# Performance work log

Hardware: AMD Instinct MI355X
Metric: run time of the kernel (lower is better)

## Reference

```python
import jax, jax.numpy as jnp
import numpy as np

EPS = 1e-5
NUM_ROUTING = 2
PC_N, PC_D = 32, 16  # primary capsules: num, dim
SD = 4               # sqrt(caps_dim) for matrix pose


def layer_norm(x, g, b):
    mu = jnp.mean(x, axis=-1, keepdims=True)
    var = jnp.mean((x - mu) ** 2, axis=-1, keepdims=True)
    return (x - mu) * jax.lax.rsqrt(var + EPS) * g + b


def conv2d(x, w, stride, pad):
    return jax.lax.conv_general_dilated(
        x, w, (stride, stride), [(pad, pad), (pad, pad)],
        dimension_numbers=('NCHW', 'OIHW', 'NCHW'))


def unfold_caps(x, k, s):
    # x: [B,N,H,W,D] -> [B,N,k,k,oh,ow,D]  (torch .unfold over H,W)
    H = x.shape[2]
    oh = (H - k) // s + 1
    idx = s * jnp.arange(oh)[:, None] + jnp.arange(k)[None, :]  # [oh,k]
    p = x[:, :, idx]            # [B,N,oh,k,W,D]
    p = p[:, :, :, :, idx]      # [B,N,oh,k,ow,k,D]
    return jnp.transpose(p, (0, 1, 3, 5, 2, 4, 6))


def caps_conv_step(val, w, stride, next_val=None):
    # val: [B,N,H,W,D]; w: [k,k,N,sd,sd,M]; inverted dot-product attention routing
    k, _, N, sd, _, M = w.shape
    u = unfold_caps(val, k, stride)              # [B,N,k,k,oh,ow,D]
    B, _, _, _, oh, ow, D = u.shape
    u = u.reshape(B, N, k, k, oh, ow, sd, sd)
    scale = 1.0 / np.sqrt(float(sd * sd))
    if next_val is None:
        # uniform query_key = softmax(zeros) = 1/M
        nv = jnp.einsum('bnklhwax,klnxdm->bmhwad', u, w) / M
    else:
        nvp = next_val.reshape(B, M, oh, ow, sd, sd)
        qk = jnp.einsum('bnklhwax,klnxdm,bmhwad->bnklmhw', u, w, nvp) * scale
        qk = jax.nn.softmax(qk, axis=4)
        nv = jnp.einsum('bnklmhw,bnklhwax,klnxdm->bmhwad', qk, u, w)
    return nv.reshape(B, M, oh, ow, sd * sd)


def caps_fc_step(val, w, next_val=None):
    # val: [B,n,D]; w: [n,sd,sd,M]
    n, sd, _, M = w.shape
    B = val.shape[0]
    u = val.reshape(B, n, sd, sd)
    scale = 1.0 / np.sqrt(float(sd * sd))
    if next_val is None:
        nv = jnp.einsum('bnax,nxdm->bmad', u, w) / M
    else:
        nvp = next_val.reshape(B, M, sd, sd)
        qk = jnp.einsum('bnax,nxdm,bmad->bnm', u, w, nvp) * scale
        qk = jax.nn.softmax(qk, axis=2)
        nv = jnp.einsum('bnm,bnax,nxdm->bmad', qk, u, w)
    return nv.reshape(B, M, sd * sd)


def _forward(x, bb_w, bb_b, pc_w, ln0_g, ln0_b, caps_w, ln1_g, ln1_b, fc_w, ln2_g, ln2_b):
    # simple backbone: conv stride2 + relu -> [B,128,32,32]
    c = jax.nn.relu(conv2d(x, bb_w, 2, 1) + bb_b[None, :, None, None])
    # primary capsule conv (no bias) -> [B, 512, 16, 16]
    u = conv2d(c, pc_w, 2, 1)
    B, _, H, W = u.shape
    u = jnp.transpose(u, (0, 2, 3, 1)).reshape(B, H, W, PC_N, PC_D)
    u = jnp.transpose(u, (0, 3, 1, 2, 4))  # [B,N,H,W,D]
    val = layer_norm(u, ln0_g, ln0_b)
    # CapsuleCONV layer with sequential routing (num_routing iterations)
    v = layer_norm(caps_conv_step(val, caps_w, 2), ln1_g, ln1_b)
    for _ in range(NUM_ROUTING - 1):
        v = layer_norm(caps_conv_step(val, caps_w, 2, next_val=v), ln1_g, ln1_b)
    # flatten 5D -> [B, M*oh*ow, D] exactly as torch permute(0,4,1,2,3).view(B,D,-1).permute(0,2,1)
    Bv, M, oh, ow, D = v.shape
    fc_in = jnp.transpose(v, (0, 4, 1, 2, 3)).reshape(Bv, D, M * oh * ow)
    fc_in = jnp.transpose(fc_in, (0, 2, 1))
    # final FC capsule layer (class capsules) with sequential routing
    p = layer_norm(caps_fc_step(fc_in, fc_w), ln2_g, ln2_b)
    for _ in range(NUM_ROUTING - 1):
        p = layer_norm(caps_fc_step(fc_in, fc_w, next_val=p), ln2_g, ln2_b)
    return p  # [B, 10, 16] class-capsule poses


def setup_inputs():
    key = jax.random.key(0)
    ks = jax.random.split(key, 5)
    B, C, HW = 64, 3, 64
    BB_OUT = 128
    CC_N, K = 32, 3
    CLS_N = 10
    cc_out = 7
    in_n_fc = CC_N * cc_out * cc_out  # 1568
    inp = {}
    inp['x'] = jax.random.normal(ks[0], (B, C, HW, HW), jnp.float32)
    inp['bb_w'] = jax.random.normal(ks[1], (BB_OUT, C, 3, 3), jnp.float32) * 0.1
    inp['bb_b'] = jnp.zeros((BB_OUT,), jnp.float32)
    inp['pc_w'] = jax.random.normal(ks[2], (PC_N * PC_D, BB_OUT, 3, 3), jnp.float32) * 0.05
    inp['ln0_g'] = jnp.ones((PC_D,), jnp.float32)
    inp['ln0_b'] = jnp.zeros((PC_D,), jnp.float32)
    cc_const = float(np.sqrt(CC_N / (SD * PC_N * K * K)))
    inp['caps_w'] = cc_const * jax.random.normal(ks[3], (K, K, PC_N, SD, SD, CC_N), jnp.float32)
    inp['ln1_g'] = jnp.ones((16,), jnp.float32)
    inp['ln1_b'] = jnp.zeros((16,), jnp.float32)
    fc_const = float(np.sqrt(CLS_N / (SD * in_n_fc)))
    inp['fc_w'] = fc_const * jax.random.normal(ks[4], (in_n_fc, SD, SD, CLS_N), jnp.float32)
    inp['ln2_g'] = jnp.ones((16,), jnp.float32)
    inp['ln2_b'] = jnp.zeros((16,), jnp.float32)
    return inp


def reference(x, bb_w, bb_b, pc_w, ln0_g, ln0_b, caps_w, ln1_g, ln1_b, fc_w, ln2_g, ln2_b):
    return _forward(x, bb_w, bb_b, pc_w, ln0_g, ln0_b, caps_w, ln1_g, ln1_b, fc_w, ln2_g, ln2_b)
```

## Files before the change

kernel.cpp:

```cpp
#include <hip/hip_runtime.h>


#define EPSLN 1e-5f

typedef short  short8 __attribute__((ext_vector_type(8)));
typedef __bf16 bf16x8 __attribute__((ext_vector_type(8)));
typedef float  f32x4  __attribute__((ext_vector_type(4)));

union Frag { short8 s; bf16x8 b; };

__device__ __forceinline__ uint4 pack_bf16_8(float4 a, float4 b) {
    union { __bf16 h[8]; uint4 u; } r;
    r.h[0] = (__bf16)a.x; r.h[1] = (__bf16)a.y;
    r.h[2] = (__bf16)a.z; r.h[3] = (__bf16)a.w;
    r.h[4] = (__bf16)b.x; r.h[5] = (__bf16)b.y;
    r.h[6] = (__bf16)b.z; r.h[7] = (__bf16)b.w;
    return r.u;
}

__device__ __forceinline__ void gld16(const void* g, void* l) {
    __builtin_amdgcn_global_load_lds(
        (const __attribute__((address_space(1))) void*)g,
        (__attribute__((address_space(3))) void*)l, 16, 0, 0);
}

__global__ __launch_bounds__(256) void k_repack_all(
        const float* __restrict__ bw,  float* __restrict__ bwT,
        const float* __restrict__ pw,  __bf16* __restrict__ wbT,
        const float* __restrict__ fw,  float* __restrict__ fwp,
        const float* __restrict__ cw,  __bf16* __restrict__ cw2,
        __bf16* __restrict__ cwB) {
    int blk = blockIdx.x;
    if (blk < 2304) {
        int i = blk * 256 + threadIdx.x;
        int oc = i / 1152, r = i % 1152;
        int ic = r / 9, tap = r % 9;
        wbT[oc * 1152 + tap * 128 + ic] = (__bf16)pw[i];
    } else if (blk < 3284) {
        int i = (blk - 2304) * 256 + threadIdx.x;
        int m = i % 10;
        int d = (i / 10) & 3;
        int x = (i / 40) & 3;
        int n = i / 160;
        fwp[(m * 1568 + n) * 16 + x * 4 + d] = fw[i];
    } else if (blk < 3860) {
        int i = (blk - 3284) * 256 + threadIdx.x;
        int m  = i & 31;
        int d  = (i >> 5) & 3;
        int x  = (i >> 7) & 3;
        int n  = (i >> 9) & 31;
        int kl = i >> 14;
        cw2[(((kl * 32 + n) * 32) + m) * 16 + x * 4 + d] = (__bf16)cw[i];
    } else if (blk < 4436) {
        int i = (blk - 3860) * 256 + threadIdx.x;
        int m  = i & 31;
        int d  = (i >> 5) & 3;
        int x  = (i >> 7) & 3;
        int n  = (i >> 9) & 31;
        int kl = i >> 14;
        cwB[(m * 4 + d) * 1152 + (n * 9 + kl) * 4 + x] = (__bf16)cw[i];
    } else {
        int i = (blk - 4436) * 256 + threadIdx.x;
        if (i < 3456) {
            int oc = i / 27, r = i % 27;
            bwT[r * 128 + oc] = bw[i];
        }
    }
}

__global__ __launch_bounds__(256) void k_conv1(const float* __restrict__ x,
                                               const float* __restrict__ bwT,
                                               const float* __restrict__ bb,
                                               __bf16* __restrict__ c2p) {
    int gid = blockIdx.x * 256 + threadIdx.x;
    int oc4 = gid & 31;
    int p   = gid >> 5;
    int w = p & 31, h = (p >> 5) & 31, b = p >> 10;
    const float* xb = x + b * 12288;
    float4 acc = *(const float4*)(bb + oc4 * 4);
    #pragma unroll
    for (int ky = 0; ky < 3; ++ky) {
        int ih = 2 * h + ky - 1;
        if ((unsigned)ih >= 64u) continue;
        #pragma unroll
        for (int kx = 0; kx < 3; ++kx) {
            int iw = 2 * w + kx - 1;
            if ((unsigned)iw >= 64u) continue;
            #pragma unroll
            for (int ic = 0; ic < 3; ++ic) {
                float in = xb[(ic * 64 + ih) * 64 + iw];
                float4 wv = *(const float4*)(bwT + (ic * 9 + ky * 3 + kx) * 128 + oc4 * 4);
                acc.x = fmaf(in, wv.x, acc.x);
                acc.y = fmaf(in, wv.y, acc.y);
                acc.z = fmaf(in, wv.z, acc.z);
                acc.w = fmaf(in, wv.w, acc.w);
            }
        }
    }
    union { __bf16 h4[4]; unsigned long long ull; } r;
    r.h4[0] = (__bf16)fmaxf(acc.x, 0.f);
    r.h4[1] = (__bf16)fmaxf(acc.y, 0.f);
    r.h4[2] = (__bf16)fmaxf(acc.z, 0.f);
    r.h4[3] = (__bf16)fmaxf(acc.w, 0.f);
    *(unsigned long long*)(c2p + ((b * 34 + h + 1) * 34 + (w + 1)) * 128 + oc4 * 4) = r.ull;
}

__global__ __launch_bounds__(256) void k_conv2_mfma(const __bf16* __restrict__ c2p,
                                                    const __bf16* __restrict__ wbT,
                                                    const float* __restrict__ g,
                                                    const float* __restrict__ bt,
                                                    float* __restrict__ val) {
    __shared__ unsigned short sA[2][128 * 32];
    __shared__ unsigned short sB[2][64 * 32];

    const int t = threadIdx.x;
    const int mblk = blockIdx.x >> 3, nblk = blockIdx.x & 7;
    const int pbase = mblk * 128, ocbase = nblk * 64;
    const int b = pbase >> 8;

    const int kc8 = (t & 3) * 8;
    const int r0 = t >> 2;
    const int oh0 = ((pbase + r0) >> 4) & 15, ow0 = (pbase + r0) & 15;
    const int oh1 = ((pbase + r0 + 64) >> 4) & 15, ow1 = (pbase + r0 + 64) & 15;

    const unsigned short* cb = (const unsigned short*)c2p + (size_t)b * 147968;
    const unsigned short* ws = (const unsigned short*)wbT
                               + (ocbase + (t >> 2)) * 1152 + kc8;

    const int lane = t & 63, wid = t >> 6;
    const int lo = lane & 15, hi = lane >> 4;

    f32x4 acc[2][4];
    #pragma unroll
    for (int fr = 0; fr < 2; ++fr)
        #pragma unroll
        for (int fc = 0; fc < 4; ++fc)
            acc[fr][fc] = (f32x4){0.f, 0.f, 0.f, 0.f};

    auto stage = [&](int buf, int ks) {
        int tap = ks / 4, ic0 = (ks % 4) * 32;
        int ty = tap / 3, tx = tap % 3;
        gld16(cb + ((2 * oh0 + ty) * 34 + (2 * ow0 + tx)) * 128 + ic0 + kc8,
              &sA[buf][(unsigned)t * 8]);
        gld16(cb + ((2 * oh1 + ty) * 34 + (2 * ow1 + tx)) * 128 + ic0 + kc8,
              &sA[buf][((unsigned)t + 256) * 8]);
        gld16(ws + ks * 32, &sB[buf][(unsigned)t * 8]);
    };

    stage(0, 0);
    __syncthreads();

    for (int ks = 0; ks < 36; ++ks) {
        const int cur = ks & 1;
        if (ks + 1 < 36) stage(cur ^ 1, ks + 1);
        Frag af0, af1, bf[4];
        af0.s = *(const short8*)&sA[cur][(wid * 32 + lo) * 32 + hi * 8];
        af1.s = *(const short8*)&sA[cur][(wid * 32 + 16 + lo) * 32 + hi * 8];
        #pragma unroll
        for (int fc = 0; fc < 4; ++fc)
            bf[fc].s = *(const short8*)&sB[cur][(fc * 16 + lo) * 32 + hi * 8];
        #pragma unroll
        for (int fc = 0; fc < 4; ++fc) {
            acc[0][fc] = __builtin_amdgcn_mfma_f32_16x16x32_bf16(
                af0.b, bf[fc].b, acc[0][fc], 0, 0, 0);
            acc[1][fc] = __builtin_amdgcn_mfma_f32_16x16x32_bf16(
                af1.b, bf[fc].b, acc[1][fc], 0, 0, 0);
        }
        __syncthreads();
    }

    const float gv = g[lo], bv = bt[lo];
    #pragma unroll
    for (int fr = 0; fr < 2; ++fr) {
        #pragma unroll
        for (int fc = 0; fc < 4; ++fc) {
            const int n = (ocbase >> 4) + fc;
            #pragma unroll
            for (int j = 0; j < 4; ++j) {
                float v = acc[fr][fc][j];
                float s1 = v, s2 = v * v;
                #pragma unroll
                for (int off = 1; off < 16; off <<= 1) {
                    s1 += __shfl_xor(s1, off);
                    s2 += __shfl_xor(s2, off);
                }
                float mu  = s1 * (1.f / 16.f);
                float var = s2 * (1.f / 16.f) - mu * mu;
                float rs  = rsqrtf(var + EPSLN);
                float o   = (v - mu) * rs * gv + bv;
                int p  = pbase + wid * 32 + fr * 16 + hi * 4 + j;
                int oh = (p >> 4) & 15, ow = p & 15;
                val[(((b * 32 + n) * 16 + oh) * 16 + ow) * 16 + lo] = o;
            }
        }
    }
}

__global__ __launch_bounds__(256) void k_nv1_mfma(const float* __restrict__ val,
                                                  const __bf16* __restrict__ cwB,
                                                  float* __restrict__ nv1g) {
    __shared__ unsigned short sA[128 * 32];
    __shared__ unsigned short sB[64 * 32];

    const int t = threadIdx.x;
    const int mblk = blockIdx.x >> 1, nblk = blockIdx.x & 1;
    const int pbase = mblk * 128, ocbase = nblk * 64;

    const float* vbase[2];
    #pragma unroll
    for (int u = 0; u < 2; ++u) {
        int r = pbase + (t >> 2) + u * 64;
        int site = r >> 2, a = r & 3;
        int b = site / 49, hw = site % 49;
        int h = hw / 7, w = hw % 7;
        vbase[u] = val + (size_t)b * 131072 + (2 * h) * 256 + (2 * w) * 16 + a * 4;
    }
    const unsigned short* wsrc = (const unsigned short*)cwB
                                 + (ocbase + (t >> 2)) * 1152 + (t & 3) * 8;

    const int lane = t & 63, wid = t >> 6;
    const int lo = lane & 15, hi = lane >> 4;

    f32x4 acc[2][4];
    #pragma unroll
    for (int fr = 0; fr < 2; ++fr)
        #pragma unroll
        for (int fc = 0; fc < 4; ++fc)
            acc[fr][fc] = (f32x4){0.f, 0.f, 0.f, 0.f};

    auto itemoff = [](int i) {
        int n = i / 9, kl = i % 9;
        return n * 4096 + (kl / 3) * 256 + (kl % 3) * 16;
    };

    {
        int i0 = (t & 3) * 2;
        int o0 = itemoff(i0), o1 = itemoff(i0 + 1);
        uint4 a0 = pack_bf16_8(*(const float4*)(vbase[0] + o0),
                               *(const float4*)(vbase[0] + o1));
        uint4 a1 = pack_bf16_8(*(const float4*)(vbase[1] + o0),
                               *(const float4*)(vbase[1] + o1));
        uint4 b0 = *(const uint4*)(wsrc);
        *(uint4*)&sA[(unsigned)t * 8]         = a0;
        *(uint4*)&sA[((unsigned)t + 256) * 8] = a1;
        *(uint4*)&sB[(unsigned)t * 8]         = b0;
        __syncthreads();
    }

    for (int ks = 0; ks < 36; ++ks) {
        uint4 a0, a1, b0;
        const bool pre = (ks + 1) < 36;
        if (pre) {
            int i0 = (ks + 1) * 8 + (t & 3) * 2;
            int o0 = itemoff(i0), o1 = itemoff(i0 + 1);
            a0 = pack_bf16_8(*(const float4*)(vbase[0] + o0),
                             *(const float4*)(vbase[0] + o1));
            a1 = pack_bf16_8(*(const float4*)(vbase[1] + o0),
                             *(const float4*)(vbase[1] + o1));
            b0 = *(const uint4*)(wsrc + (ks + 1) * 32);
        }
        Frag af0, af1, bf[4];
        af0.s = *(const short8*)&sA[(wid * 32 + lo) * 32 + hi * 8];
        af1.s = *(const short8*)&sA[(wid * 32 + 16 + lo) * 32 + hi * 8];
        #pragma unroll
        for (int fc = 0; fc < 4; ++fc)
            bf[fc].s = *(const short8*)&sB[(fc * 16 + lo) * 32 + hi * 8];
        #pragma unroll
        for (int fc = 0; fc < 4; ++fc) {
            acc[0][fc] = __builtin_amdgcn_mfma_f32_16x16x32_bf16(
                af0.b, bf[fc].b, acc[0][fc], 0, 0, 0);
            acc[1][fc] = __builtin_amdgcn_mfma_f32_16x16x32_bf16(
                af1.b, bf[fc].b, acc[1][fc], 0, 0, 0);
        }
        __syncthreads();
        if (pre) {
            *(uint4*)&sA[(unsigned)t * 8]         = a0;
            *(uint4*)&sA[((unsigned)t + 256) * 8] = a1;
            *(uint4*)&sB[(unsigned)t * 8]         = b0;
        }
        __syncthreads();
    }

    #pragma unroll
    for (int fr = 0; fr < 2; ++fr)
        #pragma unroll
        for (int fc = 0; fc < 4; ++fc)
            #pragma unroll
            for (int j = 0; j < 4; ++j) {
                int row = pbase + wid * 32 + fr * 16 + hi * 4 + j;
                int col = ocbase + fc * 16 + lo;
                nv1g[row * 128 + col] = acc[fr][fc][j];
            }
}

__global__ __launch_bounds__(256) void k_capsfused(const float* __restrict__ val,
                                                   const __bf16* __restrict__ cw2,
                                                   const float* __restrict__ nv1g,
                                                   const float* __restrict__ g,
                                                   const float* __restrict__ bt,
                                                   float* __restrict__ vout) {
    int bb = blockIdx.x / 49;
    int hw = blockIdx.x % 49;
    int h = hw / 7, w = hw % 7;

    __shared__ float4 uloc4[2][1152];
    __shared__ float  v1s[2][512];
    float* wred = (float*)uloc4;

    for (int t = threadIdx.x; t < 2304; t += 256) {
        int s  = t >= 1152;
        int tt = t - s * 1152;
        int f  = tt & 3;
        int kl = (tt >> 2) % 9;
        int n  = tt / 36;
        int k = kl / 3, l = kl % 3;
        int b = bb + s * 32;
        uloc4[s][tt] = *(const float4*)(val +
            (((b * 32 + n) * 16 + (2 * h + k)) * 16 + (2 * w + l)) * 16 + f * 4);
    }

    const int lane  = threadIdx.x & 31;
    const int grpid = threadIdx.x >> 5;
    const int wid   = threadIdx.x >> 6;
    const bool half0 = (threadIdx.x & 32) == 0;

    float nvp[2][16];
    #pragma unroll
    for (int s = 0; s < 2; ++s) {
        int site = (bb + s * 32) * 49 + hw;
        #pragma unroll
        for (int a = 0; a < 4; ++a) {
            float4 q = *(const float4*)(nv1g + (site * 4 + a) * 128 + lane * 4);
            nvp[s][a * 4 + 0] = q.x * (1.f / 32.f);
            nvp[s][a * 4 + 1] = q.y * (1.f / 32.f);
            nvp[s][a * 4 + 2] = q.z * (1.f / 32.f);
            nvp[s][a * 4 + 3] = q.w * (1.f / 32.f);
        }
        float mu = 0.f;
        #pragma unroll
        for (int j = 0; j < 16; ++j) mu += nvp[s][j];
        mu *= (1.f / 16.f);
        float var = 0.f;
        #pragma unroll
        for (int j = 0; j < 16; ++j) { float d = nvp[s][j] - mu; var += d * d; }
        var *= (1.f / 16.f);
        float rs = rsqrtf(var + EPSLN);
        #pragma unroll
        for (int j = 0; j < 16; ++j)
            nvp[s][j] = (nvp[s][j] - mu) * rs * g[j] + bt[j];
    }

    float nvacc[2][16];
    #pragma unroll
    for (int s = 0; s < 2; ++s)
        #pragma unroll
        for (int j = 0; j < 16; ++j) nvacc[s][j] = 0.f;

    __syncthreads();

    {
        uint4 wq0, wq1;
        {
            int n = grpid / 9, kl = grpid % 9;
            const uint4* wb = (const uint4*)(cw2 + (((kl * 32 + n) * 32) + lane) * 16);
            wq0 = wb[0]; wq1 = wb[1];
        }
        for (int it = grpid; it < 288; it += 8) {
            int nit = it + 8;
            uint4 nq0 = wq0, nq1 = wq1;
            if (nit < 288) {
                int n = nit / 9, kl = nit % 9;
                const uint4* wb = (const uint4*)(cw2 + (((kl * 32 + n) * 32) + lane) * 16);
                nq0 = wb[0]; nq1 = wb[1];
            }
            float cwv[16];
            {
                union { uint4 u; __bf16 hh[8]; } qa, qb;
                qa.u = wq0; qb.u = wq1;
                #pragma unroll
                for (int j = 0; j < 8; ++j) {
                    cwv[j] = (float)qa.hh[j]; cwv[8 + j] = (float)qb.hh[j];
                }
            }
            #pragma unroll
            for (int s = 0; s < 2; ++s) {
                float u16[16];
                #pragma unroll
                for (int f = 0; f < 4; ++f) {
                    float4 t4 = uloc4[s][it * 4 + f];
                    u16[f * 4 + 0] = t4.x; u16[f * 4 + 1] = t4.y;
                    u16[f * 4 + 2] = t4.z; u16[f * 4 + 3] = t4.w;
                }
                float votes[16];
                #pragma unroll
                for (int a = 0; a < 4; ++a)
                    #pragma unroll
                    for (int d = 0; d < 4; ++d) {
                        float v = 0.f;
                        #pragma unroll
                        for (int x = 0; x < 4; ++x)
                            v = fmaf(u16[a * 4 + x], cwv[x * 4 + d], v);
                        votes[a * 4 + d] = v;
                    }
                float qk = 0.f;
                #pragma unroll
                for (int j = 0; j < 16; ++j) qk = fmaf(votes[j], nvp[s][j], qk);
                qk *= 0.25f;
                float e = __expf(fminf(qk, 60.f));
                float sm = e;
                #pragma unroll
                for (int off = 1; off < 32; off <<= 1) sm += __shfl_xor(sm, off);
                float qv = e * __builtin_amdgcn_rcpf(sm);
                #pragma unroll
                for (int j = 0; j < 16; ++j) nvacc[s][j] = fmaf(qv, votes[j], nvacc[s][j]);
            }
            wq0 = nq0; wq1 = nq1;
        }
    }

    #pragma unroll
    for (int s = 0; s < 2; ++s)
        #pragma unroll
        for (int j = 0; j < 16; ++j)
            nvacc[s][j] += __shfl_xor(nvacc[s][j], 32);
    #pragma unroll
    for (int s = 0; s < 2; ++s) {
        __syncthreads();
        if (half0) {
            #pragma unroll
            for (int j = 0; j < 16; ++j) wred[wid * 544 + lane * 17 + j] = nvacc[s][j];
        }
        __syncthreads();
        for (int o = threadIdx.x; o < 512; o += 256) {
            int mm = o >> 4, j = o & 15;
            float sum = wred[0 * 544 + mm * 17 + j] + wred[1 * 544 + mm * 17 + j]
                      + wred[2 * 544 + mm * 17 + j] + wred[3 * 544 + mm * 17 + j];
            v1s[s][o] = sum;
        }
    }
    __syncthreads();
    if (threadIdx.x < 64) {
        int s = threadIdx.x >> 5, m = threadIdx.x & 31;
        int b = bb + s * 32;
        float v16[16], mu = 0.f;
        #pragma unroll
        for (int j = 0; j < 16; ++j) { v16[j] = v1s[s][m * 16 + j]; mu += v16[j]; }
        mu *= (1.f / 16.f);
        float var = 0.f;
        #pragma unroll
        for (int j = 0; j < 16; ++j) { float t = v16[j] - mu; var += t * t; }
        var *= (1.f / 16.f);
        float rs = rsqrtf(var + EPSLN);
        float o16[16];
        #pragma unroll
        for (int j = 0; j < 16; ++j) o16[j] = (v16[j] - mu) * rs * g[j] + bt[j];
        float4* dst = (float4*)(vout + (((b * 32 + m) * 7 + h) * 7 + w) * 16);
        dst[0] = make_float4(o16[0],  o16[1],  o16[2],  o16[3]);
        dst[1] = make_float4(o16[4],  o16[5],  o16[6],  o16[7]);
        dst[2] = make_float4(o16[8],  o16[9],  o16[10], o16[11]);
        dst[3] = make_float4(o16[12], o16[13], o16[14], o16[15]);
    }
}

__global__ __launch_bounds__(256) void k_fc1(const float* __restrict__ fin,
                                             const float* __restrict__ fwp,
                                             const float* __restrict__ g,
                                             const float* __restrict__ bt,
                                             float* __restrict__ p) {
    int b = blockIdx.x / 10, m = blockIdx.x % 10;
    const float* fb = fin + b * 1568 * 16;
    const float* wb = fwp + m * 1568 * 16;
    float acc[16];
    #pragma unroll
    for (int j = 0; j < 16; ++j) acc[j] = 0.f;

    for (int n = threadIdx.x; n < 1568; n += 256) {
        const float4* u4 = (const float4*)(fb + n * 16);
        const float4* w4 = (const float4*)(wb + n * 16);
        float u16[16], w16[16];
        #pragma unroll
        for (int f = 0; f < 4; ++f) {
            float4 a = u4[f], bq = w4[f];
            u16[f * 4 + 0] = a.x;  u16[f * 4 + 1] = a.y;
            u16[f * 4 + 2] = a.z;  u16[f * 4 + 3] = a.w;
            w16[f * 4 + 0] = bq.x; w16[f * 4 + 1] = bq.y;
            w16[f * 4 + 2] = bq.z; w16[f * 4 + 3] = bq.w;
        }
        #pragma unroll
        for (int a = 0; a < 4; ++a)
            #pragma unroll
            for (int d = 0; d < 4; ++d) {
                float s = acc[a * 4 + d];
                #pragma unroll
                for (int x = 0; x < 4; ++x)
                    s = fmaf(u16[a * 4 + x], w16[x * 4 + d], s);
                acc[a * 4 + d] = s;
            }
    }
    #pragma unroll
    for (int j = 0; j < 16; ++j)
        #pragma unroll
        for (int off = 1; off < 64; off <<= 1)
            acc[j] += __shfl_xor(acc[j], off);

    __shared__ float red[4][16];
    int wid = threadIdx.x >> 6, ln = threadIdx.x & 63;
    if (ln == 0) {
        #pragma unroll
        for (int j = 0; j < 16; ++j) red[wid][j] = acc[j];
    }
    __syncthreads();
    if (threadIdx.x < 16) {
        int j = threadIdx.x;
        float s = (red[0][j] + red[1][j] + red[2][j] + red[3][j]) * 0.1f;
        float mu = s;
        #pragma unroll
        for (int off = 1; off < 16; off <<= 1) mu += __shfl_xor(mu, off);
        mu *= (1.f / 16.f);
        float t = s - mu;
        float var = t * t;
        #pragma unroll
        for (int off = 1; off < 16; off <<= 1) var += __shfl_xor(var, off);
        var *= (1.f / 16.f);
        float rs = rsqrtf(var + EPSLN);
        p[(b * 10 + m) * 16 + j] = t * rs * g[j] + bt[j];
    }
}

__global__ __launch_bounds__(256) void k_fc2_part(const float* __restrict__ fin,
                                                  const float* __restrict__ fw,
                                                  const float* __restrict__ p,
                                                  float* __restrict__ part) {
    int b = blockIdx.x >> 4, slice = blockIdx.x & 15;
    int ad    = threadIdx.x & 15;
    int grpid = threadIdx.x >> 4;
    int a = ad >> 2, d = ad & 3;

    float pv[10];
    #pragma unroll
    for (int m = 0; m < 10; ++m) pv[m] = p[(b * 10 + m) * 16 + ad];

    float acc[10];
    #pragma unroll
    for (int m = 0; m < 10; ++m) acc[m] = 0.f;

    const float* fb = fin + b * 1568 * 16;
    int nbase = slice * 98;
    for (int n = nbase + grpid; n < nbase + 98; n += 16) {
        float4 u4 = *(const float4*)(fb + n * 16 + a * 4);
        const float* wb = fw + n * 160 + d * 10;
        float votes[10];
        #pragma unroll
        for (int m = 0; m < 10; ++m)
            votes[m] = u4.x * wb[m] + u4.y * wb[40 + m] +
                       u4.z * wb[80 + m] + u4.w * wb[120 + m];
        float qk[10];
        #pragma unroll
        for (int m = 0; m < 10; ++m) {
            float t = votes[m] * pv[m];
            #pragma unroll
            for (int off = 1; off < 16; off <<= 1) t += __shfl_xor(t, off);
            qk[m] = t * 0.25f;
        }
        float mx = qk[0];
        #pragma unroll
        for (int m = 1; m < 10; ++m) mx = fmaxf(mx, qk[m]);
        float e[10], s = 0.f;
        #pragma unroll
        for (int m = 0; m < 10; ++m) { e[m] = __expf(qk[m] - mx); s += e[m]; }
        float inv = 1.f / s;
        #pragma unroll
        for (int m = 0; m < 10; ++m) acc[m] = fmaf(e[m] * inv, votes[m], acc[m]);
    }

    __shared__ float red[16][16][10];
    #pragma unroll
    for (int m = 0; m < 10; ++m) red[grpid][ad][m] = acc[m];
    __syncthreads();

    if (threadIdx.x < 160) {
        int m = threadIdx.x / 16, j = threadIdx.x % 16;
        float s = 0.f;
        #pragma unroll
        for (int gg = 0; gg < 16; ++gg) s += red[gg][j][m];
        part[(b * 16 + slice) * 160 + m * 16 + j] = s;
    }
}

__global__ __launch_bounds__(256) void k_fc2_fin(const float* __restrict__ part,
                                                 const float* __restrict__ g,
                                                 const float* __restrict__ bt,
                                                 float* __restrict__ out) {
    int b = blockIdx.x;
    if (threadIdx.x >= 160) return;
    int m = threadIdx.x / 16, j = threadIdx.x % 16;
    float s = 0.f;
    #pragma unroll
    for (int sl = 0; sl < 16; ++sl)
        s += part[(b * 16 + sl) * 160 + m * 16 + j];
    float mu = s;
    #pragma unroll
    for (int off = 1; off < 16; off <<= 1) mu += __shfl_xor(mu, off);
    mu *= (1.f / 16.f);
    float t = s - mu;
    float var = t * t;
    #pragma unroll
    for (int off = 1; off < 16; off <<= 1) var += __shfl_xor(var, off);
    var *= (1.f / 16.f);
    float rs = rsqrtf(var + EPSLN);
    out[(b * 10 + m) * 16 + j] = t * rs * g[j] + bt[j];
}

extern "C" void kernel_launch(void* const* d_in, const int* in_sizes, int n_in,
                              void* d_out, int out_size, void* d_ws, size_t ws_size,
                              hipStream_t stream) {
    const float* x    = (const float*)d_in[0];
    const float* bbw  = (const float*)d_in[1];
    const float* bbb  = (const float*)d_in[2];
    const float* pcw  = (const float*)d_in[3];
    const float* ln0g = (const float*)d_in[4];
    const float* ln0b = (const float*)d_in[5];
    const float* cwt  = (const float*)d_in[6];
    const float* ln1g = (const float*)d_in[7];
    const float* ln1b = (const float*)d_in[8];
    const float* fw   = (const float*)d_in[9];
    const float* ln2g = (const float*)d_in[10];
    const float* ln2b = (const float*)d_in[11];
    float* outp = (float*)d_out;

    float* ws = (float*)d_ws;
    __bf16* c2p  = (__bf16*)ws;
    __bf16* wbT  = (__bf16*)(ws + 4734976);
    float*  bwT  = ws + 5029888;
    float*  val  = ws + 5033344;
    float*  v2   = ws + 13421952;
    float*  fwp  = ws + 15027584;
    float*  p    = ws + 15278464;
    __bf16* cw2  = (__bf16*)(ws + 15288704);
    __bf16* cwB  = (__bf16*)(ws + 15362432);
    float*  nv1g = ws + 15436160;
    float*  part = val;

    hipMemsetAsync(c2p, 0, (size_t)9469952 * 2, stream);
    k_repack_all <<<4450, 256, 0, stream>>>(bbw, bwT, pcw, wbT, fw, fwp, cwt, cw2, cwB);
    k_conv1      <<<8192, 256, 0, stream>>>(x, bwT, bbb, c2p);
    k_conv2_mfma <<<1024, 256, 0, stream>>>(c2p, wbT, ln0g, ln0b, val);
    k_nv1_mfma   <<<196,  256, 0, stream>>>(val, cwB, nv1g);
    k_capsfused  <<<1568, 256, 0, stream>>>(val, cw2, nv1g, ln1g, ln1b, v2);
    k_fc1        <<<640, 256, 0, stream>>>(v2, fwp, ln2g, ln2b, p);
    k_fc2_part   <<<1024, 256, 0, stream>>>(v2, fw, p, part);
    k_fc2_fin    <<<64, 256, 0, stream>>>(part, ln2g, ln2b, outp);
}
```

Before: 276.7 us.

## Tile conv1 rows in LDS, halve nv1 tile, swizzle capsfused blocks

conv1 now gives each block one output row: it stages the three needed input rows per channel in shared memory and keeps all 27 weight vectors in registers, with each thread computing four output columns. The nv1 GEMM tile drops from 128 to 64 rows so twice as many blocks launch, which should fill the GPU better. capsfused block indices are swizzled so neighbouring blocks hit different batch/site groups, presumably to spread them across XCDs or caches. The costs are higher register pressure in conv1 and less B-tile reuse in nv1.

```diff
diff --git a/kernel.cpp b/kernel.cpp
--- a/kernel.cpp
+++ b/kernel.cpp
@@ -72,37 +72,54 @@
                                                const float* __restrict__ bwT,
                                                const float* __restrict__ bb,
                                                __bf16* __restrict__ c2p) {
-    int gid = blockIdx.x * 256 + threadIdx.x;
-    int oc4 = gid & 31;
-    int p   = gid >> 5;
-    int w = p & 31, h = (p >> 5) & 31, b = p >> 10;
-    const float* xb = x + b * 12288;
-    float4 acc = *(const float4*)(bb + oc4 * 4);
-    #pragma unroll
-    for (int ky = 0; ky < 3; ++ky) {
-        int ih = 2 * h + ky - 1;
-        if ((unsigned)ih >= 64u) continue;
-        #pragma unroll
-        for (int kx = 0; kx < 3; ++kx) {
-            int iw = 2 * w + kx - 1;
-            if ((unsigned)iw >= 64u) continue;
+    __shared__ float xs[3][3][66];
+
+    int b = blockIdx.x >> 5, h = blockIdx.x & 31;
+    for (int i = threadIdx.x; i < 594; i += 256) {
+        int iw = i % 66;
+        int r  = (i / 66) % 3;
+        int ic = i / 198;
+        int ih  = 2 * h + r - 1;
+        int riw = iw - 1;
+        float v = 0.f;
+        if ((unsigned)ih < 64u && (unsigned)riw < 64u)
+            v = x[((b * 3 + ic) * 64 + ih) * 64 + riw];
+        xs[ic][r][iw] = v;
+    }
+    __syncthreads();
+
+    int oc4 = threadIdx.x & 31, wq = threadIdx.x >> 5;
+    float4 wv[27];
+    #pragma unroll
+    for (int r = 0; r < 27; ++r)
+        wv[r] = *(const float4*)(bwT + r * 128 + oc4 * 4);
+    float4 bias = *(const float4*)(bb + oc4 * 4);
+
+    #pragma unroll
+    for (int q = 0; q < 4; ++q) {
+        int w = wq + q * 8;
+        float4 acc = bias;
+        #pragma unroll
+        for (int ky = 0; ky < 3; ++ky)
             #pragma unroll
-            for (int ic = 0; ic < 3; ++ic) {
-                float in = xb[(ic * 64 + ih) * 64 + iw];
-                float4 wv = *(const float4*)(bwT + (ic * 9 + ky * 3 + kx) * 128 + oc4 * 4);
-                acc.x = fmaf(in, wv.x, acc.x);
-                acc.y = fmaf(in, wv.y, acc.y);
-                acc.z = fmaf(in, wv.z, acc.z);
-                acc.w = fmaf(in, wv.w, acc.w);
-            }
-        }
-    }
-    union { __bf16 h4[4]; unsigned long long ull; } r;
-    r.h4[0] = (__bf16)fmaxf(acc.x, 0.f);
-    r.h4[1] = (__bf16)fmaxf(acc.y, 0.f);
-    r.h4[2] = (__bf16)fmaxf(acc.z, 0.f);
-    r.h4[3] = (__bf16)fmaxf(acc.w, 0.f);
-    *(unsigned long long*)(c2p + ((b * 34 + h + 1) * 34 + (w + 1)) * 128 + oc4 * 4) = r.ull;
+            for (int kx = 0; kx < 3; ++kx)
+                #pragma unroll
+                for (int ic = 0; ic < 3; ++ic) {
+                    float in = xs[ic][ky][2 * w + kx];
+                    float4 ww = wv[ic * 9 + ky * 3 + kx];
+                    acc.x = fmaf(in, ww.x, acc.x);
+                    acc.y = fmaf(in, ww.y, acc.y);
+                    acc.z = fmaf(in, ww.z, acc.z);
+                    acc.w = fmaf(in, ww.w, acc.w);
+                }
+        union { __bf16 h4[4]; unsigned long long ull; } r;
+        r.h4[0] = (__bf16)fmaxf(acc.x, 0.f);
+        r.h4[1] = (__bf16)fmaxf(acc.y, 0.f);
+        r.h4[2] = (__bf16)fmaxf(acc.z, 0.f);
+        r.h4[3] = (__bf16)fmaxf(acc.w, 0.f);
+        *(unsigned long long*)(c2p + ((b * 34 + h + 1) * 34 + (w + 1)) * 128 + oc4 * 4)
+            = r.ull;
+    }
 }
 
 __global__ __launch_bounds__(256) void k_conv2_mfma(const __bf16* __restrict__ c2p,
@@ -199,21 +216,20 @@
 __global__ __launch_bounds__(256) void k_nv1_mfma(const float* __restrict__ val,
                                                   const __bf16* __restrict__ cwB,
                                                   float* __restrict__ nv1g) {
-    __shared__ unsigned short sA[128 * 32];
+    __shared__ unsigned short sA[64 * 32];
     __shared__ unsigned short sB[64 * 32];
 
     const int t = threadIdx.x;
     const int mblk = blockIdx.x >> 1, nblk = blockIdx.x & 1;
-    const int pbase = mblk * 128, ocbase = nblk * 64;
-
-    const float* vbase[2];
-    #pragma unroll
-    for (int u = 0; u < 2; ++u) {
-        int r = pbase + (t >> 2) + u * 64;
+    const int pbase = mblk * 64, ocbase = nblk * 64;
+
+    const float* vbase;
+    {
+        int r = pbase + (t >> 2);
         int site = r >> 2, a = r & 3;
         int b = site / 49, hw = site % 49;
         int h = hw / 7, w = hw % 7;
-        vbase[u] = val + (size_t)b * 131072 + (2 * h) * 256 + (2 * w) * 16 + a * 4;
+        vbase = val + (size_t)b * 131072 + (2 * h) * 256 + (2 * w) * 16 + a * 4;
     }
     const unsigned short* wsrc = (const unsigned short*)cwB
                                  + (ocbase + (t >> 2)) * 1152 + (t & 3) * 8;
@@ -221,12 +237,10 @@
     const int lane = t & 63, wid = t >> 6;
     const int lo = lane & 15, hi = lane >> 4;
 
-    f32x4 acc[2][4];
-    #pragma unroll
-    for (int fr = 0; fr < 2; ++fr)
-        #pragma unroll
-        for (int fc = 0; fc < 4; ++fc)
-            acc[fr][fc] = (f32x4){0.f, 0.f, 0.f, 0.f};
+    f32x4 acc[4];
+    #pragma unroll
+    for (int fc = 0; fc < 4; ++fc)
+        acc[fc] = (f32x4){0.f, 0.f, 0.f, 0.f};
 
     auto itemoff = [](int i) {
         int n = i / 9, kl = i % 9;
@@ -236,61 +250,49 @@
     {
         int i0 = (t & 3) * 2;
         int o0 = itemoff(i0), o1 = itemoff(i0 + 1);
-        uint4 a0 = pack_bf16_8(*(const float4*)(vbase[0] + o0),
-                               *(const float4*)(vbase[0] + o1));
-        uint4 a1 = pack_bf16_8(*(const float4*)(vbase[1] + o0),
-                               *(const float4*)(vbase[1] + o1));
+        uint4 a0 = pack_bf16_8(*(const float4*)(vbase + o0),
+                               *(const float4*)(vbase + o1));
         uint4 b0 = *(const uint4*)(wsrc);
-        *(uint4*)&sA[(unsigned)t * 8]         = a0;
-        *(uint4*)&sA[((unsigned)t + 256) * 8] = a1;
-        *(uint4*)&sB[(unsigned)t * 8]         = b0;
+        *(uint4*)&sA[(unsigned)t * 8] = a0;
+        *(uint4*)&sB[(unsigned)t * 8] = b0;
         __syncthreads();
     }
 
     for (int ks = 0; ks < 36; ++ks) {
-        uint4 a0, a1, b0;
+        uint4 a0, b0;
         const bool pre = (ks + 1) < 36;
         if (pre) {
             int i0 = (ks + 1) * 8 + (t & 3) * 2;
             int o0 = itemoff(i0), o1 = itemoff(i0 + 1);
-            a0 = pack_bf16_8(*(const float4*)(vbase[0] + o0),
-                             *(const float4*)(vbase[0] + o1));
-            a1 = pack_bf16_8(*(const float4*)(vbase[1] + o0),
-                             *(const float4*)(vbase[1] + o1));
+            a0 = pack_bf16_8(*(const float4*)(vbase + o0),
+                             *(const float4*)(vbase + o1));
             b0 = *(const uint4*)(wsrc + (ks + 1) * 32);
         }
-        Frag af0, af1, bf[4];
-        af0.s = *(const short8*)&sA[(wid * 32 + lo) * 32 + hi * 8];
-        af1.s = *(const short8*)&sA[(wid * 32 + 16 + lo) * 32 + hi * 8];
+        Frag af, bf[4];
+        af.s = *(const short8*)&sA[(wid * 16 + lo) * 32 + hi * 8];
         #pragma unroll
         for (int fc = 0; fc < 4; ++fc)
             bf[fc].s = *(const short8*)&sB[(fc * 16 + lo) * 32 + hi * 8];
         #pragma unroll
-        for (int fc = 0; fc < 4; ++fc) {
-            acc[0][fc] = __builtin_amdgcn_mfma_f32_16x16x32_bf16(
-                af0.b, bf[fc].b, acc[0][fc], 0, 0, 0);
-            acc[1][fc] = __builtin_amdgcn_mfma_f32_16x16x32_bf16(
-                af1.b, bf[fc].b, acc[1][fc], 0, 0, 0);
-        }
+        for (int fc = 0; fc < 4; ++fc)
+            acc[fc] = __builtin_amdgcn_mfma_f32_16x16x32_bf16(
+                af.b, bf[fc].b, acc[fc], 0, 0, 0);
         __syncthreads();
         if (pre) {
-            *(uint4*)&sA[(unsigned)t * 8]         = a0;
-            *(uint4*)&sA[((unsigned)t + 256) * 8] = a1;
-            *(uint4*)&sB[(unsigned)t * 8]         = b0;
+            *(uint4*)&sA[(unsigned)t * 8] = a0;
+            *(uint4*)&sB[(unsigned)t * 8] = b0;
         }
         __syncthreads();
     }
 
     #pragma unroll
-    for (int fr = 0; fr < 2; ++fr)
-        #pragma unroll
-        for (int fc = 0; fc < 4; ++fc)
-            #pragma unroll
-            for (int j = 0; j < 4; ++j) {
-                int row = pbase + wid * 32 + fr * 16 + hi * 4 + j;
-                int col = ocbase + fc * 16 + lo;
-                nv1g[row * 128 + col] = acc[fr][fc][j];
-            }
+    for (int fc = 0; fc < 4; ++fc)
+        #pragma unroll
+        for (int j = 0; j < 4; ++j) {
+            int row = pbase + wid * 16 + hi * 4 + j;
+            int col = ocbase + fc * 16 + lo;
+            nv1g[row * 128 + col] = acc[fc][j];
+        }
 }
 
 __global__ __launch_bounds__(256) void k_capsfused(const float* __restrict__ val,
@@ -299,8 +301,9 @@
                                                    const float* __restrict__ g,
                                                    const float* __restrict__ bt,
                                                    float* __restrict__ vout) {
-    int bb = blockIdx.x / 49;
-    int hw = blockIdx.x % 49;
+    int swz = (blockIdx.x & 7) * 196 + (blockIdx.x >> 3);
+    int bb = swz / 49;
+    int hw = swz % 49;
     int h = hw / 7, w = hw % 7;
 
     __shared__ float4 uloc4[2][1152];
@@ -643,9 +646,9 @@
 
     hipMemsetAsync(c2p, 0, (size_t)9469952 * 2, stream);
     k_repack_all <<<4450, 256, 0, stream>>>(bbw, bwT, pcw, wbT, fw, fwp, cwt, cw2, cwB);
-    k_conv1      <<<8192, 256, 0, stream>>>(x, bwT, bbb, c2p);
+    k_conv1      <<<2048, 256, 0, stream>>>(x, bwT, bbb, c2p);
     k_conv2_mfma <<<1024, 256, 0, stream>>>(c2p, wbT, ln0g, ln0b, val);
-    k_nv1_mfma   <<<196,  256, 0, stream>>>(val, cwB, nv1g);
+    k_nv1_mfma   <<<392,  256, 0, stream>>>(val, cwB, nv1g);
     k_capsfused  <<<1568, 256, 0, stream>>>(val, cw2, nv1g, ln1g, ln1b, v2);
     k_fc1        <<<640, 256, 0, stream>>>(v2, fwp, ln2g, ln2b, p);
     k_fc2_part   <<<1024, 256, 0, stream>>>(v2, fw, p, part);
```

Result: faster. 246.1 us (-11.1%).
